# Optimization experiments

Hardware: AMD Instinct MI355X
Metric: run time of the kernel (lower is better)

## Reference

```python
import jax, jax.numpy as jnp
import numpy as np

B, S, E, H, NCTX = 32, 4095, 1024, 16, 4096  # cache len S, new seq_len = S+1
HD = E // H

def setup_inputs() -> dict:
    key = jax.random.key(0)
    ks = jax.random.split(key, 8)
    return {
        "hidden_states": jax.random.normal(ks[0], (B, 1, E), jnp.float32),
        "key_cache": jax.random.normal(ks[1], (B, S, E), jnp.float32),
        "value_cache": jax.random.normal(ks[2], (B, S, E), jnp.float32),
        "attention_mask": jnp.ones((B, S + 1), jnp.int32),
        "c_attn_w": jax.random.normal(ks[3], (E, 3 * E), jnp.float32) * 0.02,
        "c_attn_b": jax.random.normal(ks[4], (3 * E,), jnp.float32) * 0.02,
        "c_proj_w": jax.random.normal(ks[5], (E, E), jnp.float32) * 0.02,
        "c_proj_b": jax.random.normal(ks[6], (E,), jnp.float32) * 0.02,
        "attn_bias": jax.random.normal(ks[7], (NCTX, NCTX), jnp.float32) * 0.02,
    }

def reference(hidden_states, key_cache, value_cache, attention_mask,
              c_attn_w, c_attn_b, c_proj_w, c_proj_b, attn_bias):
    b, _, e = hidden_states.shape
    h, hd = H, E // H
    seq_len = key_cache.shape[1] + 1
    # fused qkv projection on the single decode token
    qkv = hidden_states[:, 0, :] @ c_attn_w + c_attn_b          # [B, 3E]
    q, k, v = jnp.split(qkv, 3, axis=-1)                         # each [B, E]
    # last valid position in attention_mask (index of last 1)
    rev = attention_mask[:, ::-1]
    last = attention_mask.shape[1] - jnp.argmax(rev, axis=1) - 1  # [B]
    # append zero column then scatter new k/v at per-batch last position
    zcol = jnp.zeros((b, 1, e), key_cache.dtype)
    bidx = jnp.arange(b)
    new_k = jnp.concatenate([key_cache, zcol], axis=1).at[bidx, last].set(k)   # [B, seq_len, E]
    new_v = jnp.concatenate([value_cache, zcol], axis=1).at[bidx, last].set(v)
    # multi-head attention with q_len = 1
    qh = q.reshape(b, h, hd)                                     # [B, H, hd]
    kh = new_k.reshape(b, seq_len, h, hd)                        # [B, S+1, H, hd]
    vh = new_v.reshape(b, seq_len, h, hd)
    scores = jnp.einsum('bhd,bshd->bhs', qh, kh) / jnp.sqrt(jnp.float32(hd))  # [B, H, S+1]
    scores = scores + attn_bias[0, :seq_len][None, None, :]
    scores = jnp.where(attention_mask[:, None, :] == 0, jnp.float32(-1e9), scores)
    w = jax.nn.softmax(scores, axis=-1)
    ctx = jnp.einsum('bhs,bshd->bhd', w, vh).reshape(b, 1, e)    # [B, 1, E]
    out = ctx @ c_proj_w + c_proj_b                               # resid_dropout is eval no-op
    return out, new_k, new_v
```

## Files before the change

### kernel.cpp

```cpp
#include <hip/hip_runtime.h>
#include <hip/hip_bf16.h>

#define BATCH 32
#define S_LEN 4095
#define SEQ   4096
#define E_DIM 1024
#define NH    16
#define HD    64
#define CHUNK 128
#define NCHUNK (SEQ / CHUNK)

__global__ __launch_bounds__(256) void last_kernel(const int* __restrict__ mask,
                                                   int* __restrict__ lastbuf) {
    int b = blockIdx.x;
    int t = threadIdx.x;
    int best = -1;
    for (int s = t; s < SEQ; s += 256)
        if (mask[b * SEQ + s] != 0) best = max(best, s);
    __shared__ int red[256];
    red[t] = best;
    __syncthreads();
    for (int o = 128; o > 0; o >>= 1) {
        if (t < o) red[t] = max(red[t], red[t + o]);
        __syncthreads();
    }
    if (t == 0) lastbuf[b] = (red[0] < 0) ? (SEQ - 1) : red[0];
}

__global__ __launch_bounds__(256) void qkv_kernel(const float* __restrict__ hs,
                                                  const float* __restrict__ W,
                                                  const float* __restrict__ bias,
                                                  float* __restrict__ qkv) {
    int b = blockIdx.y;
    int j = blockIdx.x * 256 + threadIdx.x;
    __shared__ float h[E_DIM];
    for (int i = threadIdx.x; i < E_DIM; i += 256) h[i] = hs[b * E_DIM + i];
    __syncthreads();
    float acc = bias[j];
    for (int i = 0; i < E_DIM; ++i) acc = fmaf(h[i], W[(size_t)i * 3072 + j], acc);
    qkv[b * 3072 + j] = acc;
}

__global__ __launch_bounds__(256) void attn_partial_kernel(
    const float* __restrict__ kcache, const float* __restrict__ vcache,
    const int* __restrict__ mask, const float* __restrict__ bias,
    const float* __restrict__ qkv, const int* __restrict__ lastbuf,
    float* __restrict__ newk, float* __restrict__ newv,
    float* __restrict__ pm, float* __restrict__ pl, float* __restrict__ pctx) {
    const int b = blockIdx.y;
    const int chunk = blockIdx.x;
    const int t = threadIdx.x;
    const int wave = t >> 6;
    const int lane = t & 63;
    const int head = wave * 4 + (lane >> 4);
    const int lig = lane & 15;
    const int col = head * HD + lig * 4;
    const int last = lastbuf[b];

    const float4 q4 = *(const float4*)(qkv + b * 3072 + col);
    const float4 kn4 = *(const float4*)(qkv + b * 3072 + 1024 + col);
    const float4 vn4 = *(const float4*)(qkv + b * 3072 + 2048 + col);

    const float* kb = kcache + (size_t)b * S_LEN * E_DIM;
    const float* vb = vcache + (size_t)b * S_LEN * E_DIM;
    float* nkb = newk + (size_t)b * SEQ * E_DIM;
    float* nvb = newv + (size_t)b * SEQ * E_DIM;
    const int* mb = mask + b * SEQ;

    float m = -3.0e38f, l = 0.f;
    float4 acc = make_float4(0.f, 0.f, 0.f, 0.f);

    const int s0 = chunk * CHUNK;
    for (int r = 0; r < CHUNK; ++r) {
        const int s = s0 + r;
        float4 kk, vv;
        if (s == last) {
            kk = kn4; vv = vn4;
        } else if (s < S_LEN) {
            kk = *(const float4*)(kb + (size_t)s * E_DIM + col);
            vv = *(const float4*)(vb + (size_t)s * E_DIM + col);
        } else {
            kk = make_float4(0.f, 0.f, 0.f, 0.f);
            vv = kk;
        }
        *(float4*)(nkb + (size_t)s * E_DIM + col) = kk;
        *(float4*)(nvb + (size_t)s * E_DIM + col) = vv;

        float p = kk.x * q4.x + kk.y * q4.y + kk.z * q4.z + kk.w * q4.w;
        p += __shfl_xor(p, 1);
        p += __shfl_xor(p, 2);
        p += __shfl_xor(p, 4);
        p += __shfl_xor(p, 8);
        float score = p * 0.125f + bias[s];
        if (mb[s] == 0) score = -1.0e9f;

        const float mnew = fmaxf(m, score);
        const float sc = __expf(m - mnew);
        const float w = __expf(score - mnew);
        l = l * sc + w;
        acc.x = acc.x * sc + w * vv.x;
        acc.y = acc.y * sc + w * vv.y;
        acc.z = acc.z * sc + w * vv.z;
        acc.w = acc.w * sc + w * vv.w;
        m = mnew;
    }

    const int pidx = (b * NH + head) * NCHUNK + chunk;
    if (lig == 0) { pm[pidx] = m; pl[pidx] = l; }
    *(float4*)(pctx + (size_t)pidx * HD + lig * 4) = acc;
}

__global__ __launch_bounds__(256) void reduce_kernel(const float* __restrict__ pm,
                                                     const float* __restrict__ pl,
                                                     const float* __restrict__ pctx,
                                                     float* __restrict__ ctxout) {
    const int gw = (blockIdx.x * blockDim.x + threadIdx.x) >> 6;
    const int lane = threadIdx.x & 63;
    if (gw >= BATCH * NH) return;
    float mg = -3.0e38f;
    for (int c = 0; c < NCHUNK; ++c) mg = fmaxf(mg, pm[gw * NCHUNK + c]);
    float lacc = 0.f, cacc = 0.f;
    for (int c = 0; c < NCHUNK; ++c) {
        const float e = __expf(pm[gw * NCHUNK + c] - mg);
        lacc = fmaf(pl[gw * NCHUNK + c], e, lacc);
        cacc = fmaf(pctx[(size_t)(gw * NCHUNK + c) * HD + lane], e, cacc);
    }
    ctxout[gw * HD + lane] = cacc / lacc;
}

__global__ __launch_bounds__(256) void proj_kernel(const float* __restrict__ ctx,
                                                   const float* __restrict__ W,
                                                   const float* __restrict__ bias,
                                                   float* __restrict__ out) {
    int b = blockIdx.y;
    int j = blockIdx.x * 256 + threadIdx.x;
    __shared__ float h[E_DIM];
    for (int i = threadIdx.x; i < E_DIM; i += 256) h[i] = ctx[b * E_DIM + i];
    __syncthreads();
    float acc = bias[j];
    for (int i = 0; i < E_DIM; ++i) acc = fmaf(h[i], W[(size_t)i * E_DIM + j], acc);
    out[b * E_DIM + j] = acc;
}

extern "C" void kernel_launch(void* const* d_in, const int* in_sizes, int n_in,
                              void* d_out, int out_size, void* d_ws, size_t ws_size,
                              hipStream_t stream) {
    const float* hs      = (const float*)d_in[0];
    const float* kcache  = (const float*)d_in[1];
    const float* vcache  = (const float*)d_in[2];
    const int*   mask    = (const int*)d_in[3];
    const float* attn_w  = (const float*)d_in[4];
    const float* attn_b  = (const float*)d_in[5];
    const float* proj_w  = (const float*)d_in[6];
    const float* proj_b  = (const float*)d_in[7];
    const float* bias0   = (const float*)d_in[8];

    float* out0 = (float*)d_out;
    float* newk = out0 + (size_t)BATCH * E_DIM;
    float* newv = newk + (size_t)BATCH * SEQ * E_DIM;

    float* ws = (float*)d_ws;
    float* qkv     = ws;
    float* ctxbuf  = qkv + 98304;
    float* pm      = ctxbuf + 32768;
    float* pl      = pm + 16384;
    float* pctx    = pl + 16384;
    int*   lastbuf = (int*)(pctx + 1048576);

    last_kernel<<<dim3(BATCH), dim3(256), 0, stream>>>(mask, lastbuf);
    qkv_kernel<<<dim3(12, BATCH), dim3(256), 0, stream>>>(hs, attn_w, attn_b, qkv);
    attn_partial_kernel<<<dim3(NCHUNK, BATCH), dim3(256), 0, stream>>>(
        kcache, vcache, mask, bias0, qkv, lastbuf, newk, newv, pm, pl, pctx);
    reduce_kernel<<<dim3((BATCH * NH * 64 + 255) / 256), dim3(256), 0, stream>>>(
        pm, pl, pctx, ctxbuf);
    proj_kernel<<<dim3(4, BATCH), dim3(256), 0, stream>>>(ctxbuf, proj_w, proj_b, out0);
}
```

Measured before the change: 536.7 us.

## Use nontemporal vector loads/stores, unrolled clean-chunk path, and adaptive chunk count

The attention kernel now uses nontemporal 128-bit loads and stores for the KV cache copy. It adds a fast path for chunks that contain neither the inserted token nor the tail, which batches four rows of loads and stores before the compute so more memory requests are in flight. When the workspace is large enough it switches to 64-row chunks, doubling the grid to 2048 blocks for better occupancy, at the cost of more partials for the reduce kernel. The GEMV loops in the QKV and projection kernels get an unroll hint.

```diff
diff --git a/kernel.cpp b/kernel.cpp
--- a/kernel.cpp
+++ b/kernel.cpp
@@ -1,5 +1,7 @@
 #include <hip/hip_runtime.h>
 #include <hip/hip_bf16.h>
+
+typedef float f32x4 __attribute__((ext_vector_type(4)));
 
 #define BATCH 32
 #define S_LEN 4095
@@ -7,8 +9,13 @@
 #define E_DIM 1024
 #define NH    16
 #define HD    64
-#define CHUNK 128
-#define NCHUNK (SEQ / CHUNK)
+
+__device__ __forceinline__ f32x4 ntload4(const float* p) {
+    return __builtin_nontemporal_load((const f32x4*)p);
+}
+__device__ __forceinline__ void ntstore4(float* p, f32x4 v) {
+    __builtin_nontemporal_store(v, (f32x4*)p);
+}
 
 __global__ __launch_bounds__(256) void last_kernel(const int* __restrict__ mask,
                                                    int* __restrict__ lastbuf) {
@@ -37,16 +44,19 @@
     for (int i = threadIdx.x; i < E_DIM; i += 256) h[i] = hs[b * E_DIM + i];
     __syncthreads();
     float acc = bias[j];
+    #pragma unroll 8
     for (int i = 0; i < E_DIM; ++i) acc = fmaf(h[i], W[(size_t)i * 3072 + j], acc);
     qkv[b * 3072 + j] = acc;
 }
 
+template <int CHUNK_T>
 __global__ __launch_bounds__(256) void attn_partial_kernel(
     const float* __restrict__ kcache, const float* __restrict__ vcache,
     const int* __restrict__ mask, const float* __restrict__ bias,
     const float* __restrict__ qkv, const int* __restrict__ lastbuf,
     float* __restrict__ newk, float* __restrict__ newv,
     float* __restrict__ pm, float* __restrict__ pl, float* __restrict__ pctx) {
+    constexpr int NCHUNK_T = SEQ / CHUNK_T;
     const int b = blockIdx.y;
     const int chunk = blockIdx.x;
     const int t = threadIdx.x;
@@ -57,9 +67,9 @@
     const int col = head * HD + lig * 4;
     const int last = lastbuf[b];
 
-    const float4 q4 = *(const float4*)(qkv + b * 3072 + col);
-    const float4 kn4 = *(const float4*)(qkv + b * 3072 + 1024 + col);
-    const float4 vn4 = *(const float4*)(qkv + b * 3072 + 2048 + col);
+    const f32x4 q4 = *(const f32x4*)(qkv + b * 3072 + col);
+    const f32x4 kn4 = *(const f32x4*)(qkv + b * 3072 + 1024 + col);
+    const f32x4 vn4 = *(const f32x4*)(qkv + b * 3072 + 2048 + col);
 
     const float* kb = kcache + (size_t)b * S_LEN * E_DIM;
     const float* vb = vcache + (size_t)b * S_LEN * E_DIM;
@@ -68,62 +78,96 @@
     const int* mb = mask + b * SEQ;
 
     float m = -3.0e38f, l = 0.f;
-    float4 acc = make_float4(0.f, 0.f, 0.f, 0.f);
-
-    const int s0 = chunk * CHUNK;
-    for (int r = 0; r < CHUNK; ++r) {
-        const int s = s0 + r;
-        float4 kk, vv;
-        if (s == last) {
-            kk = kn4; vv = vn4;
-        } else if (s < S_LEN) {
-            kk = *(const float4*)(kb + (size_t)s * E_DIM + col);
-            vv = *(const float4*)(vb + (size_t)s * E_DIM + col);
-        } else {
-            kk = make_float4(0.f, 0.f, 0.f, 0.f);
-            vv = kk;
+    f32x4 acc = (f32x4){0.f, 0.f, 0.f, 0.f};
+
+    const int s0 = chunk * CHUNK_T;
+    const bool clean = (s0 + CHUNK_T <= S_LEN) && (last < s0 || last >= s0 + CHUNK_T);
+
+    if (clean) {
+        for (int r = 0; r < CHUNK_T; r += 4) {
+            f32x4 kk[4], vv[4];
+            #pragma unroll
+            for (int u = 0; u < 4; ++u) {
+                const size_t off = (size_t)(s0 + r + u) * E_DIM + col;
+                kk[u] = ntload4(kb + off);
+                vv[u] = ntload4(vb + off);
+            }
+            #pragma unroll
+            for (int u = 0; u < 4; ++u) {
+                const size_t off = (size_t)(s0 + r + u) * E_DIM + col;
+                ntstore4(nkb + off, kk[u]);
+                ntstore4(nvb + off, vv[u]);
+            }
+            #pragma unroll
+            for (int u = 0; u < 4; ++u) {
+                const int s = s0 + r + u;
+                float p = kk[u][0] * q4[0] + kk[u][1] * q4[1] + kk[u][2] * q4[2] + kk[u][3] * q4[3];
+                p += __shfl_xor(p, 1);
+                p += __shfl_xor(p, 2);
+                p += __shfl_xor(p, 4);
+                p += __shfl_xor(p, 8);
+                float score = p * 0.125f + bias[s];
+                if (mb[s] == 0) score = -1.0e9f;
+                const float mnew = fmaxf(m, score);
+                const float sc = __expf(m - mnew);
+                const float w = __expf(score - mnew);
+                l = l * sc + w;
+                acc = acc * sc + vv[u] * w;
+                m = mnew;
+            }
         }
-        *(float4*)(nkb + (size_t)s * E_DIM + col) = kk;
-        *(float4*)(nvb + (size_t)s * E_DIM + col) = vv;
-
-        float p = kk.x * q4.x + kk.y * q4.y + kk.z * q4.z + kk.w * q4.w;
-        p += __shfl_xor(p, 1);
-        p += __shfl_xor(p, 2);
-        p += __shfl_xor(p, 4);
-        p += __shfl_xor(p, 8);
-        float score = p * 0.125f + bias[s];
-        if (mb[s] == 0) score = -1.0e9f;
-
-        const float mnew = fmaxf(m, score);
-        const float sc = __expf(m - mnew);
-        const float w = __expf(score - mnew);
-        l = l * sc + w;
-        acc.x = acc.x * sc + w * vv.x;
-        acc.y = acc.y * sc + w * vv.y;
-        acc.z = acc.z * sc + w * vv.z;
-        acc.w = acc.w * sc + w * vv.w;
-        m = mnew;
-    }
-
-    const int pidx = (b * NH + head) * NCHUNK + chunk;
+    } else {
+        for (int r = 0; r < CHUNK_T; ++r) {
+            const int s = s0 + r;
+            f32x4 kk, vv;
+            if (s == last) {
+                kk = kn4; vv = vn4;
+            } else if (s < S_LEN) {
+                kk = ntload4(kb + (size_t)s * E_DIM + col);
+                vv = ntload4(vb + (size_t)s * E_DIM + col);
+            } else {
+                kk = (f32x4){0.f, 0.f, 0.f, 0.f};
+                vv = kk;
+            }
+            ntstore4(nkb + (size_t)s * E_DIM + col, kk);
+            ntstore4(nvb + (size_t)s * E_DIM + col, vv);
+
+            float p = kk[0] * q4[0] + kk[1] * q4[1] + kk[2] * q4[2] + kk[3] * q4[3];
+            p += __shfl_xor(p, 1);
+            p += __shfl_xor(p, 2);
+            p += __shfl_xor(p, 4);
+            p += __shfl_xor(p, 8);
+            float score = p * 0.125f + bias[s];
+            if (mb[s] == 0) score = -1.0e9f;
+            const float mnew = fmaxf(m, score);
+            const float sc = __expf(m - mnew);
+            const float w = __expf(score - mnew);
+            l = l * sc + w;
+            acc = acc * sc + vv * w;
+            m = mnew;
+        }
+    }
+
+    const int pidx = (b * NH + head) * NCHUNK_T + chunk;
     if (lig == 0) { pm[pidx] = m; pl[pidx] = l; }
-    *(float4*)(pctx + (size_t)pidx * HD + lig * 4) = acc;
+    *(f32x4*)(pctx + (size_t)pidx * HD + lig * 4) = acc;
 }
 
 __global__ __launch_bounds__(256) void reduce_kernel(const float* __restrict__ pm,
                                                      const float* __restrict__ pl,
                                                      const float* __restrict__ pctx,
-                                                     float* __restrict__ ctxout) {
+                                                     float* __restrict__ ctxout,
+                                                     int nchunk) {
     const int gw = (blockIdx.x * blockDim.x + threadIdx.x) >> 6;
     const int lane = threadIdx.x & 63;
     if (gw >= BATCH * NH) return;
     float mg = -3.0e38f;
-    for (int c = 0; c < NCHUNK; ++c) mg = fmaxf(mg, pm[gw * NCHUNK + c]);
+    for (int c = 0; c < nchunk; ++c) mg = fmaxf(mg, pm[gw * nchunk + c]);
     float lacc = 0.f, cacc = 0.f;
-    for (int c = 0; c < NCHUNK; ++c) {
-        const float e = __expf(pm[gw * NCHUNK + c] - mg);
-        lacc = fmaf(pl[gw * NCHUNK + c], e, lacc);
-        cacc = fmaf(pctx[(size_t)(gw * NCHUNK + c) * HD + lane], e, cacc);
+    for (int c = 0; c < nchunk; ++c) {
+        const float e = __expf(pm[gw * nchunk + c] - mg);
+        lacc = fmaf(pl[gw * nchunk + c], e, lacc);
+        cacc = fmaf(pctx[(size_t)(gw * nchunk + c) * HD + lane], e, cacc);
     }
     ctxout[gw * HD + lane] = cacc / lacc;
 }
@@ -138,6 +182,7 @@
     for (int i = threadIdx.x; i < E_DIM; i += 256) h[i] = ctx[b * E_DIM + i];
     __syncthreads();
     float acc = bias[j];
+    #pragma unroll 8
     for (int i = 0; i < E_DIM; ++i) acc = fmaf(h[i], W[(size_t)i * E_DIM + j], acc);
     out[b * E_DIM + j] = acc;
 }
@@ -159,19 +204,28 @@
     float* newk = out0 + (size_t)BATCH * E_DIM;
     float* newv = newk + (size_t)BATCH * SEQ * E_DIM;
 
+    const size_t need64 = (size_t)(98304 + 32768 + 2 * (512 * 64) + (size_t)512 * 64 * 64 + 32) * 4;
+    const bool use64 = ws_size >= need64;
+    const int NCH = use64 ? 64 : 32;
+
     float* ws = (float*)d_ws;
     float* qkv     = ws;
     float* ctxbuf  = qkv + 98304;
     float* pm      = ctxbuf + 32768;
-    float* pl      = pm + 16384;
-    float* pctx    = pl + 16384;
-    int*   lastbuf = (int*)(pctx + 1048576);
+    float* pl      = pm + 512 * NCH;
+    float* pctx    = pl + 512 * NCH;
+    int*   lastbuf = (int*)(pctx + (size_t)512 * NCH * 64);
 
     last_kernel<<<dim3(BATCH), dim3(256), 0, stream>>>(mask, lastbuf);
     qkv_kernel<<<dim3(12, BATCH), dim3(256), 0, stream>>>(hs, attn_w, attn_b, qkv);
-    attn_partial_kernel<<<dim3(NCHUNK, BATCH), dim3(256), 0, stream>>>(
-        kcache, vcache, mask, bias0, qkv, lastbuf, newk, newv, pm, pl, pctx);
+    if (use64) {
+        attn_partial_kernel<64><<<dim3(64, BATCH), dim3(256), 0, stream>>>(
+            kcache, vcache, mask, bias0, qkv, lastbuf, newk, newv, pm, pl, pctx);
+    } else {
+        attn_partial_kernel<128><<<dim3(32, BATCH), dim3(256), 0, stream>>>(
+            kcache, vcache, mask, bias0, qkv, lastbuf, newk, newv, pm, pl, pctx);
+    }
     reduce_kernel<<<dim3((BATCH * NH * 64 + 255) / 256), dim3(256), 0, stream>>>(
-        pm, pl, pctx, ctxbuf);
+        pm, pl, pctx, ctxbuf, NCH);
     proj_kernel<<<dim3(4, BATCH), dim3(256), 0, stream>>>(ctxbuf, proj_w, proj_b, out0);
 }
```

Result: slower. 547.6 us (+2.0%).
